# Kernel tuning notes

Measured on AMD Instinct MI355X. Metric: run time of the kernel, lower is better.

Reference implementation:

```python
import jax, jax.numpy as jnp
import numpy as np

CH = 512
NH = 8
EPS = 1e-5

def setup_inputs() -> dict:
    key = jax.random.key(0)
    ks = jax.random.split(key, 7)
    x = jax.random.normal(ks[0], (1, CH, 64, 64), dtype=jnp.float32)
    norm_w = jnp.ones((CH,), jnp.float32)
    norm_b = jnp.zeros((CH,), jnp.float32)
    s1 = 1.0 / np.sqrt(CH)
    qkv_w = jax.random.uniform(ks[1], (3 * CH, CH), jnp.float32, -s1, s1)
    qkv_b = jax.random.uniform(ks[2], (3 * CH,), jnp.float32, -s1, s1)
    proj_w = jax.random.uniform(ks[3], (CH, CH), jnp.float32, -s1, s1)
    proj_b = jax.random.uniform(ks[4], (CH,), jnp.float32, -s1, s1)
    return {"x": x, "norm_w": norm_w, "norm_b": norm_b, "qkv_w": qkv_w,
            "qkv_b": qkv_b, "proj_w": proj_w, "proj_b": proj_b}

def _forward(x, norm_w, norm_b, qkv_w, qkv_b, proj_w, proj_b):
    B, C, H, W = x.shape
    G = 32
    # GroupNorm(32, C) + SiLU
    xg = x.reshape(B, G, C // G, H, W)
    mu = jnp.mean(xg, axis=(2, 3, 4), keepdims=True)
    var = jnp.var(xg, axis=(2, 3, 4), keepdims=True)
    h = ((xg - mu) * jax.lax.rsqrt(var + EPS)).reshape(B, C, H, W)
    h = h * norm_w[None, :, None, None] + norm_b[None, :, None, None]
    h = jax.nn.silu(h)
    N = H * W
    h = h.reshape(B, C, N)
    # qkv 1x1 conv == channel matmul
    qkv = jnp.einsum('oc,bcn->bon', qkv_w, h) + qkv_b[None, :, None]
    q, k, v = jnp.split(qkv, 3, axis=1)  # each (B, C, N)
    d = C // NH
    # faithful to torch: transpose(1,2) then row-major reshape
    q = q.transpose(0, 2, 1).reshape(B * NH, N, d)
    k = k.transpose(0, 2, 1).reshape(B * NH, N, d)
    v = v.transpose(0, 2, 1).reshape(B * NH, N, d)
    scale = d ** (-0.5)
    attn = jax.nn.softmax(jnp.einsum('bnd,bmd->bnm', q, k) * scale, axis=-1)
    out = jnp.einsum('bnm,bmd->bnd', attn, v)
    out = out.reshape(B, N, C).transpose(0, 2, 1)  # (B, C, N)
    out = jnp.einsum('oc,bcn->bon', proj_w, out) + proj_b[None, :, None]
    return x + out.reshape(B, C, H, W)

def reference(x, norm_w, norm_b, qkv_w, qkv_b, proj_w, proj_b):
    return _forward(x, norm_w, norm_b, qkv_w, qkv_b, proj_w, proj_b)
```

## Files before the change

kernel.cpp:

```cpp
#include <hip/hip_runtime.h>

typedef __attribute__((ext_vector_type(8)))  short s16x8;
typedef __attribute__((ext_vector_type(4)))  float f32x4;
typedef __attribute__((ext_vector_type(16))) float f32x16;
typedef __attribute__((ext_vector_type(4)))  unsigned int u32x4;

#define CHN 512
#define NSP 4096

__device__ __forceinline__ ushort f2b(float f){
  unsigned u = __builtin_bit_cast(unsigned, f);
  u = (u + 0x7fffu + ((u >> 16) & 1u)) >> 16;
  return (ushort)u;
}
__device__ __forceinline__ float b2f(ushort u){
  return __builtin_bit_cast(float, ((unsigned)u) << 16);
}

__device__ __forceinline__ s16x8 ldfrag(const void* p){
  return *reinterpret_cast<const s16x8*>(p);
}

__device__ __forceinline__ f32x4 mfma16(s16x8 a, s16x8 b, f32x4 c){
  return __builtin_amdgcn_mfma_f32_16x16x32_bf16(a, b, c, 0, 0, 0);
}
__device__ __forceinline__ f32x16 mfma32(s16x8 a, s16x8 b, f32x16 c){
  return __builtin_amdgcn_mfma_f32_32x32x16_bf16(a, b, c, 0, 0, 0);
}
__device__ __forceinline__ unsigned cvtpk(float lo, float hi){
  unsigned r;
  asm("v_cvt_pk_bf16_f32 %0, %1, %2" : "=v"(r) : "v"(lo), "v"(hi));
  return r;
}
__device__ __forceinline__ void gload16(const void* g, void* l){
  __builtin_amdgcn_global_load_lds(
      (const __attribute__((address_space(1))) unsigned int*)g,
      (__attribute__((address_space(3))) unsigned int*)l, 16, 0, 0);
}
__device__ __forceinline__ ushort4 f4b(float4 v){
  ushort4 o;
  o.x = f2b(v.x); o.y = f2b(v.y); o.z = f2b(v.z); o.w = f2b(v.w);
  return o;
}

__global__ __launch_bounds__(256) void prep(const float4* __restrict__ qkvw, const float4* __restrict__ projw,
                                            const float* __restrict__ x,
                                            ushort4* __restrict__ Wq, ushort4* __restrict__ Wp,
                                            float* __restrict__ part){
  int b = blockIdx.x;
  if (b < 768){
    int i = b*256 + threadIdx.x;
    Wq[i] = f4b(qkvw[i]);
  } else if (b < 1024){
    int i = (b-768)*256 + threadIdx.x;
    Wp[i] = f4b(projw[i]);
  } else {
    int pb = b - 1024;
    const float4* p = reinterpret_cast<const float4*>(x + (size_t)pb * 8192);
    float s = 0.f, s2 = 0.f;
    #pragma unroll
    for (int i = 0; i < 8; ++i){
      float4 v = p[threadIdx.x + i*256];
      s  += v.x + v.y + v.z + v.w;
      s2 += v.x*v.x + v.y*v.y + v.z*v.z + v.w*v.w;
    }
    #pragma unroll
    for (int off = 32; off > 0; off >>= 1){ s += __shfl_down(s, off); s2 += __shfl_down(s2, off); }
    __shared__ float ls[4], ls2[4];
    int wv = threadIdx.x >> 6;
    if ((threadIdx.x & 63) == 0){ ls[wv] = s; ls2[wv] = s2; }
    __syncthreads();
    if (threadIdx.x == 0){
      part[pb*2]     = ls[0]+ls[1]+ls[2]+ls[3];
      part[pb*2 + 1] = ls2[0]+ls2[1]+ls2[2]+ls2[3];
    }
  }
}

__global__ __launch_bounds__(256) void norm_apply(const float* __restrict__ x, const float* __restrict__ part,
                                                  const float* __restrict__ nw, const float* __restrict__ nb,
                                                  ushort* __restrict__ h_t){
  __shared__ float tile[64][65];
  __shared__ float smu[32], srs[32];
  if (threadIdx.x < 32){
    int g = threadIdx.x;
    float s = 0.f, s2 = 0.f;
    #pragma unroll
    for (int i = 0; i < 8; ++i){ s += part[(g*8+i)*2]; s2 += part[(g*8+i)*2+1]; }
    float mu  = s * (1.f/65536.f);
    float var = s2 * (1.f/65536.f) - mu*mu;
    smu[g] = mu;
    srs[g] = rsqrtf(var + 1e-5f);
  }
  __syncthreads();
  int ct0 = (blockIdx.x >> 6) << 6;
  int nt0 = (blockIdx.x & 63) << 6;
  int tc = threadIdx.x >> 6;
  int tn = threadIdx.x & 63;
  #pragma unroll
  for (int rr = 0; rr < 16; ++rr){
    int cl = rr*4 + tc;
    int c  = ct0 + cl;
    float v  = x[(size_t)c * NSP + nt0 + tn];
    float hn = (v - smu[c >> 4]) * srs[c >> 4] * nw[c] + nb[c];
    float sv = hn / (1.f + __expf(-hn));
    tile[tn][cl] = sv;
  }
  __syncthreads();
  #pragma unroll
  for (int rr = 0; rr < 16; ++rr){
    int nl = rr*4 + tc;
    h_t[(size_t)(nt0 + nl) * CHN + ct0 + tn] = f2b(tile[nl][tn]);
  }
}

template<int MODE, int BM, int BN>
__global__ __launch_bounds__(256) void gemm_tn(
    const ushort* __restrict__ A, const ushort* __restrict__ Bw,
    const float* __restrict__ bias, const float* __restrict__ xres,
    ushort* __restrict__ qS, ushort* __restrict__ kF, ushort* __restrict__ vF,
    float* __restrict__ outF)
{
  constexpr int RW = BM/2, CW = BN/2;
  constexpr int MI = RW/16, NJ = CW/16;
  constexpr int NL = BM/64 + BN/64;
  __shared__ __align__(16) ushort As[4][BM*32];
  __shared__ __align__(16) ushort Bs[4][BN*32];
  int tid = threadIdx.x;
  int lane = tid & 63, wv = tid >> 6;
  int lr = lane & 15, lg = lane >> 4;
  int wr = wv >> 1, wc = wv & 1;
  int nbB = blockIdx.x * BM;
  int obB = blockIdx.y * BN;
  int nb = nbB + wr*RW, ob = obB + wc*CW;
  f32x4 acc[MI][NJ] = {};

  int sswz = (tid & 3) ^ ((tid >> 2) & 3);
  const ushort* Ag = A  + (size_t)(nbB + (tid>>2))*CHN + sswz*8;
  const ushort* Bg = Bw + (size_t)(obB + (tid>>2))*CHN + sswz*8;
  int rdswz = (lg ^ (lr & 3)) * 8;

  #define GSTAGE(BUF, KK) {                                                    \
    _Pragma("unroll") for (int ii = 0; ii < BM/64; ++ii)                       \
      gload16(Ag + (size_t)ii*64*CHN + (KK), &As[BUF][ii*2048 + tid*8]);       \
    _Pragma("unroll") for (int ii = 0; ii < BN/64; ++ii)                       \
      gload16(Bg + (size_t)ii*64*CHN + (KK), &Bs[BUF][ii*2048 + tid*8]); }

  #define VWAIT() {                                                            \
    if (NL == 3)      asm volatile("s_waitcnt vmcnt(6)" ::: "memory");         \
    else              asm volatile("s_waitcnt vmcnt(4)" ::: "memory"); }

  GSTAGE(0, 0);
  GSTAGE(1, 32);
  GSTAGE(2, 64);
  VWAIT();
  __syncthreads();
  for (int ks = 0; ks < 16; ++ks){
    if (ks + 3 < 16) GSTAGE((ks+3)&3, (ks+3)*32);
    int cb = ks & 3;
    s16x8 af[MI], bf[NJ];
    #pragma unroll
    for (int t = 0; t < MI; ++t) af[t] = *(const s16x8*)&As[cb][(wr*RW + lr + t*16)*32 + rdswz];
    #pragma unroll
    for (int t = 0; t < NJ; ++t) bf[t] = *(const s16x8*)&Bs[cb][(wc*CW + lr + t*16)*32 + rdswz];
    #pragma unroll
    for (int i = 0; i < MI; ++i)
      #pragma unroll
      for (int j = 0; j < NJ; ++j)
        acc[i][j] = mfma16(af[i], bf[j], acc[i][j]);
    VWAIT();
    __syncthreads();
  }
  #undef GSTAGE
  #undef VWAIT

  if (MODE == 0){
    #pragma unroll
    for (int j = 0; j < NJ; ++j){
      int o = ob + j*16 + lr;
      float bs = bias[o];
      int sec = o >> 9;
      int co  = o & 511;
      int bb = co >> 6, dd = co & 63;
      if (sec == 0){
        const float qsc = 0.18033688011112042f;
        #pragma unroll
        for (int i = 0; i < MI; ++i){
          int n0 = nb + i*16 + lg*4;
          int hh = n0 >> 9, aa = n0 & 511;
          size_t base = ((size_t)((hh<<3)+bb)*512 + aa)*64 + dd;
          #pragma unroll
          for (int r = 0; r < 4; ++r)
            qS[base + (size_t)r*64] = f2b((acc[i][j][r] + bs) * qsc);
        }
      } else if (sec == 1){
        int s = dd >> 4, khi = (dd >> 3) & 1, off = dd & 7;
        #pragma unroll
        for (int i = 0; i < MI; ++i){
          int n0 = nb + i*16 + lg*4;
          int hh = n0 >> 9, aa = n0 & 511;
          int T = bb*16 + (aa >> 5);
          size_t widx = ((((size_t)hh*128 + T)*4 + s)*64 + (aa & 31) + 32*khi)*8 + off;
          #pragma unroll
          for (int r = 0; r < 4; ++r)
            kF[widx + (size_t)r*8] = f2b(acc[i][j][r] + bs);
        }
      } else {
        int l31v = dd & 31, fh = dd >> 5;
        #pragma unroll
        for (int i = 0; i < MI; ++i){
          int n0 = nb + i*16 + lg*4;
          int hh = n0 >> 9, aa = n0 & 511;
          int T = bb*16 + (aa >> 5);
          int w = aa & 31;
          int f = fh*2 + (w >> 4);
          int vhi = (w >> 3) & 1, koff = w & 7;
          size_t widx = ((((size_t)hh*128 + T)*4 + f)*64 + l31v + 32*vhi)*8 + koff;
          ushort4 pk;
          pk.x = f2b(acc[i][j][0] + bs);
          pk.y = f2b(acc[i][j][1] + bs);
          pk.z = f2b(acc[i][j][2] + bs);
          pk.w = f2b(acc[i][j][3] + bs);
          *reinterpret_cast<ushort4*>(vF + widx) = pk;
        }
      }
    }
  } else {
    #pragma unroll
    for (int j = 0; j < NJ; ++j){
      int o = ob + j*16 + lr;
      float bs = bias[o];
      #pragma unroll
      for (int i = 0; i < MI; ++i){
        int n0 = nb + i*16 + lg*4;
        f32x4 xr = *reinterpret_cast<const f32x4*>(xres + (size_t)o*NSP + n0);
        f32x4 ov;
        #pragma unroll
        for (int r = 0; r < 4; ++r) ov[r] = acc[i][j][r] + bs + xr[r];
        *reinterpret_cast<f32x4*>(outF + (size_t)o*NSP + n0) = ov;
      }
    }
  }
}

__global__ __launch_bounds__(512) void flash9(
    const ushort* __restrict__ qS, const ushort* __restrict__ kF,
    const ushort* __restrict__ vF, ushort* __restrict__ attnT)
{
  __shared__ __align__(16) ushort ldsK[4][2][2048];
  __shared__ __align__(16) float llds[3][64];
  __shared__ __align__(16) float winv[64];
  int lane = threadIdx.x & 63, wv = threadIdx.x >> 6;
  int l31 = lane & 31, hi = lane >> 5;
  int qg = wv & 1, kvh = wv >> 1;
  int bx = (blockIdx.x & 7) * 64 + (blockIdx.x >> 3);
  int hh    = bx >> 6;
  int b1    = (bx >> 3) & 7;
  int chunk = bx & 7;
  int a0 = chunk * 64 + qg * 32;

  const ushort* qp = qS + ((size_t)((hh*8 + b1)*512) + a0 + l31)*64 + hi*8;
  s16x8 qf0 = ldfrag(qp), qf1 = ldfrag(qp+16), qf2 = ldfrag(qp+32), qf3 = ldfrag(qp+48);

  f32x16 O0 = {}, O1 = {};
  f32x4 lacc = {};
  s16x8 v0, v1, v2, v3;

  size_t tbase = (size_t)hh*262144 + (size_t)(kvh*32)*2048;

  #define STAGEK(BUF, T) {                                                     \
    const ushort* ks_ = kF + tbase + (size_t)(T)*2048 + qg*1024 + lane*8;      \
    ushort* lk_ = &ldsK[kvh][BUF][qg*1024 + lane*8];                           \
    gload16(ks_,       lk_);                                                   \
    gload16(ks_ + 512, lk_ + 512); }

  #define LOADV(T) {                                                           \
    const ushort* vp_ = vF + tbase + (size_t)(T)*2048 + lane*8;                \
    v0 = ldfrag(vp_);        v1 = ldfrag(vp_ + 512);                           \
    v2 = ldfrag(vp_ + 1024); v3 = ldfrag(vp_ + 1536); }

  #define COMPUTE(BUF) {                                                       \
    const ushort* kc = &ldsK[kvh][BUF][lane*8];                                \
    s16x8 k0 = *(const s16x8*)(kc),        k1 = *(const s16x8*)(kc +  512);    \
    s16x8 k2 = *(const s16x8*)(kc + 1024), k3 = *(const s16x8*)(kc + 1536);    \
    f32x16 S = {};                                                             \
    S = mfma32(k0, qf0, S); S = mfma32(k1, qf1, S);                            \
    S = mfma32(k2, qf2, S); S = mfma32(k3, qf3, S);                            \
    float p[16];                                                               \
    _Pragma("unroll") for (int r = 0; r < 16; ++r)                             \
      p[r] = __builtin_amdgcn_exp2f(S[r]);                                     \
    lacc[0] += (p[0]+p[1])   + (p[2]+p[3]);                                    \
    lacc[1] += (p[4]+p[5])   + (p[6]+p[7]);                                    \
    lacc[2] += (p[8]+p[9])   + (p[10]+p[11]);                                  \
    lacc[3] += (p[12]+p[13]) + (p[14]+p[15]);                                  \
    unsigned A0 = cvtpk(p[0],p[1]),  A1 = cvtpk(p[2],p[3]);                    \
    unsigned B0 = cvtpk(p[4],p[5]),  B1 = cvtpk(p[6],p[7]);                    \
    asm("v_permlane32_swap_b32 %0, %1" : "+v"(A0), "+v"(B0));                  \
    asm("v_permlane32_swap_b32 %0, %1" : "+v"(A1), "+v"(B1));                  \
    unsigned C0 = cvtpk(p[8],p[9]),  C1 = cvtpk(p[10],p[11]);                  \
    unsigned D0 = cvtpk(p[12],p[13]),D1 = cvtpk(p[14],p[15]);                  \
    asm("v_permlane32_swap_b32 %0, %1" : "+v"(C0), "+v"(D0));                  \
    asm("v_permlane32_swap_b32 %0, %1" : "+v"(C1), "+v"(D1));                  \
    u32x4 w1 = {A0, A1, B0, B1}, w2 = {C0, C1, D0, D1};                        \
    s16x8 pa1 = __builtin_bit_cast(s16x8, w1);                                 \
    s16x8 pa2 = __builtin_bit_cast(s16x8, w2);                                 \
    O0 = mfma32(pa1, v0, O0); O0 = mfma32(pa2, v1, O0);                        \
    O1 = mfma32(pa1, v2, O1); O1 = mfma32(pa2, v3, O1);                        \
  }

  STAGEK(0, 0);
  __builtin_amdgcn_sched_barrier(0);
  LOADV(0);
  asm volatile("s_waitcnt vmcnt(4)" ::: "memory");
  __syncthreads();
  int cur = 0;
  for (int t = 0; t < 32; ++t){
    if (t < 31){
      STAGEK(cur^1, t+1);
      __builtin_amdgcn_sched_barrier(0);
    }
    COMPUTE(cur);
    if (t < 31){
      LOADV(t+1);
      asm volatile("s_waitcnt vmcnt(4)" ::: "memory");
    }
    __syncthreads();
    cur ^= 1;
  }
  #undef STAGEK
  #undef LOADV
  #undef COMPUTE

  float ts = (lacc[0]+lacc[1]) + (lacc[2]+lacc[3]);
  float tu = ts, tv = ts;
  asm("v_permlane32_swap_b32 %0, %1" : "+v"(tu), "+v"(tv));
  float lrun = tu + tv;

  if (kvh < 3){
    ushort* park = &ldsK[kvh][0][0];
    #pragma unroll
    for (int g = 0; g < 4; ++g)
      #pragma unroll
      for (int r4 = 0; r4 < 4; ++r4){
        int fr = qg*32 + g*8 + hi*4 + r4;
        park[fr*64 + l31]      = f2b(O0[g*4+r4]);
        park[fr*64 + l31 + 32] = f2b(O1[g*4+r4]);
      }
    if (hi == 0) llds[kvh][qg*32 + l31] = lrun;
  }
  __syncthreads();
  if (kvh == 3){
    if (hi == 0){
      int idx = qg*32 + l31;
      winv[idx] = 1.0f / (llds[0][idx] + llds[1][idx] + llds[2][idx] + lrun);
    }
    asm volatile("s_waitcnt lgkmcnt(0)" ::: "memory");
    const ushort* p0 = &ldsK[0][0][0];
    const ushort* p1 = &ldsK[1][0][0];
    const ushort* p2 = &ldsK[2][0][0];
    size_t colBase = (size_t)b1*64 + l31;
    #pragma unroll
    for (int g = 0; g < 4; ++g){
      f32x4 iv = *reinterpret_cast<const f32x4*>(&winv[qg*32 + g*8 + hi*4]);
      #pragma unroll
      for (int r4 = 0; r4 < 4; ++r4){
        int row = g*8 + hi*4 + r4;
        int fr = qg*32 + row;
        float o0 = (b2f(p0[fr*64 + l31]) + b2f(p1[fr*64 + l31])
                  + b2f(p2[fr*64 + l31]) + O0[g*4+r4]) * iv[r4];
        float o1 = (b2f(p0[fr*64 + l31 + 32]) + b2f(p1[fr*64 + l31 + 32])
                  + b2f(p2[fr*64 + l31 + 32]) + O1[g*4+r4]) * iv[r4];
        size_t base = ((size_t)(hh*512 + a0 + row))*CHN + colBase;
        attnT[base]      = f2b(o0);
        attnT[base + 32] = f2b(o1);
      }
    }
  }
}

extern "C" void kernel_launch(void* const* d_in, const int* in_sizes, int n_in,
                              void* d_out, int out_size, void* d_ws, size_t ws_size,
                              hipStream_t stream)
{
  (void)in_sizes; (void)n_in; (void)out_size; (void)ws_size;
  const float* x     = (const float*)d_in[0];
  const float* normw = (const float*)d_in[1];
  const float* normb = (const float*)d_in[2];
  const float* qkvw  = (const float*)d_in[3];
  const float* qkvb  = (const float*)d_in[4];
  const float* projw = (const float*)d_in[5];
  const float* projb = (const float*)d_in[6];
  float* out = (float*)d_out;

  char* w = (char*)d_ws;
  ushort* h_t  = (ushort*)(w + 1024);
  ushort* Wq   = (ushort*)(w + 1024 + 4194304);
  ushort* Wp   = (ushort*)(w + 1024 + 4194304 + 1572864);
  ushort* qSb  = (ushort*)(w + 1024 + 4194304 + 1572864 + 524288);
  ushort* kFb  = qSb + 2097152;
  ushort* vFb  = kFb + 2097152;
  float*  part = (float*)(vFb + 2097152);
  ushort* attnT = h_t;

  prep<<<1280, 256, 0, stream>>>((const float4*)qkvw, (const float4*)projw, x,
                                 (ushort4*)Wq, (ushort4*)Wp, part);
  norm_apply<<<512, 256, 0, stream>>>(x, part, normw, normb, h_t);
  gemm_tn<0,128,64><<<dim3(32, 24), 256, 0, stream>>>(h_t, Wq, qkvb, nullptr, qSb, kFb, vFb, nullptr);
  flash9<<<512, 512, 0, stream>>>(qSb, kFb, vFb, attnT);
  gemm_tn<1,64,64><<<dim3(64, 8), 256, 0, stream>>>(attnT, Wp, projb, x, nullptr, nullptr, nullptr, out);
}
```

Measured before the change: 82.79 us.

## Split flash attention blocks per query group and drop per-tile block barriers

The flash attention kernel goes from 512-thread blocks covering two 32-query groups to 256-thread blocks covering one group, launched as 1024 blocks. Each wave now stages its whole K tile into its own private LDS slice, so the two __syncthreads per KV tile are removed and only the final reduction barrier stays. The aim is to cut barrier stalls and raise block-level parallelism. In exchange, K tiles are no longer shared across two query groups, which doubles K global and LDS staging traffic, and correctness now relies on per-wave vmcnt waits alone to make the LDS data visible.

```diff
diff --git a/kernel.cpp b/kernel.cpp
--- a/kernel.cpp
+++ b/kernel.cpp
@@ -243,21 +243,20 @@
   }
 }
 
-__global__ __launch_bounds__(512) void flash9(
+__global__ __launch_bounds__(256) void flash12(
     const ushort* __restrict__ qS, const ushort* __restrict__ kF,
     const ushort* __restrict__ vF, ushort* __restrict__ attnT)
 {
   __shared__ __align__(16) ushort ldsK[4][2][2048];
-  __shared__ __align__(16) float llds[3][64];
-  __shared__ __align__(16) float winv[64];
-  int lane = threadIdx.x & 63, wv = threadIdx.x >> 6;
+  __shared__ __align__(16) float llds[3][32];
+  __shared__ __align__(16) float winv[32];
+  int lane = threadIdx.x & 63, kvh = threadIdx.x >> 6;
   int l31 = lane & 31, hi = lane >> 5;
-  int qg = wv & 1, kvh = wv >> 1;
-  int bx = (blockIdx.x & 7) * 64 + (blockIdx.x >> 3);
-  int hh    = bx >> 6;
-  int b1    = (bx >> 3) & 7;
-  int chunk = bx & 7;
-  int a0 = chunk * 64 + qg * 32;
+  int bx = (blockIdx.x & 7) * 128 + (blockIdx.x >> 3);
+  int hh    = bx >> 7;
+  int b1    = (bx >> 4) & 7;
+  int chunk = bx & 15;
+  int a0 = chunk * 32;
 
   const ushort* qp = qS + ((size_t)((hh*8 + b1)*512) + a0 + l31)*64 + hi*8;
   s16x8 qf0 = ldfrag(qp), qf1 = ldfrag(qp+16), qf2 = ldfrag(qp+32), qf3 = ldfrag(qp+48);
@@ -269,10 +268,12 @@
   size_t tbase = (size_t)hh*262144 + (size_t)(kvh*32)*2048;
 
   #define STAGEK(BUF, T) {                                                     \
-    const ushort* ks_ = kF + tbase + (size_t)(T)*2048 + qg*1024 + lane*8;      \
-    ushort* lk_ = &ldsK[kvh][BUF][qg*1024 + lane*8];                           \
-    gload16(ks_,       lk_);                                                   \
-    gload16(ks_ + 512, lk_ + 512); }
+    const ushort* ks_ = kF + tbase + (size_t)(T)*2048 + lane*8;                \
+    ushort* lk_ = &ldsK[kvh][BUF][lane*8];                                     \
+    gload16(ks_,        lk_);                                                  \
+    gload16(ks_ +  512, lk_ +  512);                                           \
+    gload16(ks_ + 1024, lk_ + 1024);                                           \
+    gload16(ks_ + 1536, lk_ + 1536); }
 
   #define LOADV(T) {                                                           \
     const ushort* vp_ = vF + tbase + (size_t)(T)*2048 + lane*8;                \
@@ -312,7 +313,6 @@
   __builtin_amdgcn_sched_barrier(0);
   LOADV(0);
   asm volatile("s_waitcnt vmcnt(4)" ::: "memory");
-  __syncthreads();
   int cur = 0;
   for (int t = 0; t < 32; ++t){
     if (t < 31){
@@ -324,7 +324,6 @@
       LOADV(t+1);
       asm volatile("s_waitcnt vmcnt(4)" ::: "memory");
     }
-    __syncthreads();
     cur ^= 1;
   }
   #undef STAGEK
@@ -342,17 +341,16 @@
     for (int g = 0; g < 4; ++g)
       #pragma unroll
       for (int r4 = 0; r4 < 4; ++r4){
-        int fr = qg*32 + g*8 + hi*4 + r4;
+        int fr = g*8 + hi*4 + r4;
         park[fr*64 + l31]      = f2b(O0[g*4+r4]);
         park[fr*64 + l31 + 32] = f2b(O1[g*4+r4]);
       }
-    if (hi == 0) llds[kvh][qg*32 + l31] = lrun;
+    if (hi == 0) llds[kvh][l31] = lrun;
   }
   __syncthreads();
   if (kvh == 3){
     if (hi == 0){
-      int idx = qg*32 + l31;
-      winv[idx] = 1.0f / (llds[0][idx] + llds[1][idx] + llds[2][idx] + lrun);
+      winv[l31] = 1.0f / (llds[0][l31] + llds[1][l31] + llds[2][l31] + lrun);
     }
     asm volatile("s_waitcnt lgkmcnt(0)" ::: "memory");
     const ushort* p0 = &ldsK[0][0][0];
@@ -361,15 +359,14 @@
     size_t colBase = (size_t)b1*64 + l31;
     #pragma unroll
     for (int g = 0; g < 4; ++g){
-      f32x4 iv = *reinterpret_cast<const f32x4*>(&winv[qg*32 + g*8 + hi*4]);
+      f32x4 iv = *reinterpret_cast<const f32x4*>(&winv[g*8 + hi*4]);
       #pragma unroll
       for (int r4 = 0; r4 < 4; ++r4){
         int row = g*8 + hi*4 + r4;
-        int fr = qg*32 + row;
-        float o0 = (b2f(p0[fr*64 + l31]) + b2f(p1[fr*64 + l31])
-                  + b2f(p2[fr*64 + l31]) + O0[g*4+r4]) * iv[r4];
-        float o1 = (b2f(p0[fr*64 + l31 + 32]) + b2f(p1[fr*64 + l31 + 32])
-                  + b2f(p2[fr*64 + l31 + 32]) + O1[g*4+r4]) * iv[r4];
+        float o0 = (b2f(p0[row*64 + l31]) + b2f(p1[row*64 + l31])
+                  + b2f(p2[row*64 + l31]) + O0[g*4+r4]) * iv[r4];
+        float o1 = (b2f(p0[row*64 + l31 + 32]) + b2f(p1[row*64 + l31 + 32])
+                  + b2f(p2[row*64 + l31 + 32]) + O1[g*4+r4]) * iv[r4];
         size_t base = ((size_t)(hh*512 + a0 + row))*CHN + colBase;
         attnT[base]      = f2b(o0);
         attnT[base + 32] = f2b(o1);
@@ -406,6 +403,6 @@
                                  (ushort4*)Wq, (ushort4*)Wp, part);
   norm_apply<<<512, 256, 0, stream>>>(x, part, normw, normb, h_t);
   gemm_tn<0,128,64><<<dim3(32, 24), 256, 0, stream>>>(h_t, Wq, qkvb, nullptr, qSb, kFb, vFb, nullptr);
-  flash9<<<512, 512, 0, stream>>>(qSb, kFb, vFb, attnT);
+  flash12<<<1024, 256, 0, stream>>>(qSb, kFb, vFb, attnT);
   gemm_tn<1,64,64><<<dim3(64, 8), 256, 0, stream>>>(attnT, Wp, projb, x, nullptr, nullptr, nullptr, out);
 }
```

Result: slower. 89.20 us (+7.7%).
